# Kernel optimization log

Hardware: AMD Instinct MI355X
Metric: run time of the kernel (lower is better)

## Reference

```python
import jax, jax.numpy as jnp
import numpy as np

N_NODES = 50000
N_EDGES = 800000
D_IN = 64
D_OUT = 64


def setup_inputs() -> dict:
    key = jax.random.key(0)
    k1, k2, k3, k4 = jax.random.split(key, 4)
    x = jax.random.normal(k1, (N_NODES, D_IN), dtype=jnp.float32)
    W = jax.random.normal(k2, (D_IN, D_OUT), dtype=jnp.float32) / np.sqrt(D_IN)
    bias = jnp.zeros((D_OUT,), dtype=jnp.float32)
    # learned per-edge weights (AdaptiveEdgeWeightGNN.edge_attr, initialized from fixed_values)
    edge_weight = jax.random.uniform(k3, (N_EDGES,), dtype=jnp.float32)
    edge_index = jax.random.randint(k4, (2, N_EDGES), 0, N_NODES, dtype=jnp.int64)
    return {"x": x, "W": W, "bias": bias, "edge_weight": edge_weight, "edge_index": edge_index}


def reference(x, W, bias, edge_weight, edge_index):
    # PyG GCNConv forward: gcn_norm (add self-loops, symmetric normalization
    # using the edge weights), linear transform, gather-scale-scatter, + bias.
    N = x.shape[0]
    row = edge_index[0]  # source nodes
    col = edge_index[1]  # target nodes
    loop = jnp.arange(N, dtype=edge_index.dtype)
    row = jnp.concatenate([row, loop])
    col = jnp.concatenate([col, loop])
    ew = jnp.concatenate([edge_weight, jnp.ones((N,), dtype=edge_weight.dtype)])
    # degree from edge weights scattered onto target nodes
    deg = jax.ops.segment_sum(ew, col, num_segments=N)
    deg_inv_sqrt = jnp.where(deg > 0, jax.lax.rsqrt(deg), 0.0)
    norm = deg_inv_sqrt[row] * ew * deg_inv_sqrt[col]  # [E+N]
    xw = x @ W  # [N, D_OUT]
    msgs = xw[row] * norm[:, None]  # gather + scale
    out = jax.ops.segment_sum(msgs, col, num_segments=N)  # scatter-add
    return out + bias
```

## Files before the change

kernel.cpp:

```cpp
#include <hip/hip_runtime.h>

#define N_NODES 50000
#define N_EDGES 800000
#define D 64
#define NCHUNK 64
#define CHUNK_E (N_EDGES / NCHUNK)
#define NRANGE 4
#define RANGE_N 16384
#define PAD 8
#define REC_CAP (N_EDGES + (PAD - 1) * N_NODES)
#define NB_NODE 196
#define PLACE_BLOCKS (N_EDGES / 256)

typedef int iv4 __attribute__((ext_vector_type(4)));

__device__ __forceinline__ unsigned short f2bf(float f) {
    unsigned int u = __float_as_uint(f);
    u += 0x7FFFu + ((u >> 16) & 1u);
    return (unsigned short)(u >> 16);
}
__device__ __forceinline__ float bf2f(unsigned int s) {
    return __uint_as_float(s << 16);
}

__global__ __launch_bounds__(1024) void k_hist(const int* __restrict__ col,
                                               unsigned short* __restrict__ part,
                                               unsigned short* __restrict__ lrank) {
    __shared__ unsigned int h[RANGE_N / 2];
    int i = blockIdx.x >> 2;
    int j = blockIdx.x & 3;
    int t = threadIdx.x;
    for (int k = t; k < RANGE_N / 2; k += 1024) h[k] = 0;
    __syncthreads();
    int base = i * CHUNK_E;
    for (int e = base + t; e < base + CHUNK_E; e += 1024) {
        int c = col[e];
        if ((c >> 14) == j) {
            int local = c & (RANGE_N - 1);
            int sh = (local & 1) << 4;
            unsigned int lr = atomicAdd(&h[local >> 1], 1u << sh);
            lrank[e] = (unsigned short)((lr >> sh) & 0xffffu);
        }
    }
    __syncthreads();
    for (int k = t; k < RANGE_N; k += 1024) {
        int n = j * RANGE_N + k;
        if (n < N_NODES)
            part[(size_t)i * N_NODES + n] =
                (unsigned short)((h[k >> 1] >> ((k & 1) << 4)) & 0xffffu);
    }
}

__global__ __launch_bounds__(256) void k_scan(unsigned short* __restrict__ part,
                                              int* __restrict__ start,
                                              int* __restrict__ cnttot,
                                              int* __restrict__ partials) {
    __shared__ int s[256];
    int b = blockIdx.x, t = threadIdx.x;
    int n = b * 256 + t;
    unsigned int run = 0;
    if (n < N_NODES) {
#pragma unroll 8
        for (int i = 0; i < NCHUNK; ++i) {
            size_t idx = (size_t)i * N_NODES + n;
            unsigned int v = part[idx];
            part[idx] = (unsigned short)run;
            run += v;
        }
        cnttot[n] = (int)run;
    }
    int cnt = (n < N_NODES) ? (int)((run + PAD - 1) & ~(unsigned)(PAD - 1)) : 0;
    s[t] = cnt;
    __syncthreads();
    for (int off = 1; off < 256; off <<= 1) {
        int a = (t >= off) ? s[t - off] : 0;
        __syncthreads();
        s[t] += a;
        __syncthreads();
    }
    if (n <= N_NODES) start[n] = s[t] - cnt;
    if (t == 255) partials[b] = s[255];
}

__global__ __launch_bounds__(256) void k_scanfin(int* __restrict__ start,
                                                 const int* __restrict__ partials) {
    __shared__ int red[256];
    int b = blockIdx.x, t = threadIdx.x;
    red[t] = (t < b) ? partials[t] : 0;
    __syncthreads();
    for (int off = 128; off > 0; off >>= 1) {
        if (t < off) red[t] += red[t + off];
        __syncthreads();
    }
    int offset = red[0];
    int n = b * 256 + t;
    if (n <= N_NODES) start[n] += offset;
}

__global__ __launch_bounds__(256) void k_place(const int* __restrict__ ei,
                                               const float* __restrict__ ew,
                                               const int* __restrict__ start,
                                               const int* __restrict__ cnttot,
                                               const unsigned short* __restrict__ part,
                                               const unsigned short* __restrict__ lrank,
                                               unsigned int* __restrict__ rec) {
    int b = blockIdx.x, t = threadIdx.x;
    if (b < PLACE_BLOCKS) {
        int e = b * 256 + t;
        int c = ei[N_EDGES + e];
        int i = e / CHUNK_E;
        int pos = start[c] + (int)part[(size_t)i * N_NODES + c] + (int)lrank[e];
        rec[pos] = (unsigned int)ei[e] | ((unsigned int)f2bf(ew[e]) << 16);
    } else {
        int n = (b - PLACE_BLOCKS) * 256 + t;
        if (n < N_NODES) {
            int j = start[n] + cnttot[n];
            int j1 = start[n + 1];
            for (; j < j1; ++j) rec[j] = 0u;
        }
    }
}

__global__ __launch_bounds__(256) void k_deg(const int* __restrict__ start,
                                             const unsigned int* __restrict__ rec,
                                             float* __restrict__ dis) {
    int wave = threadIdx.x >> 6;
    int lane = threadIdx.x & 63;
    int n = blockIdx.x * 4 + wave;
    int j0 = start[n], j1 = start[n + 1];
    float s = 0.0f;
    for (int j = j0 + lane; j < j1; j += 64) s += bf2f(rec[j] >> 16);
    for (int off = 32; off > 0; off >>= 1) s += __shfl_down(s, off);
    if (lane == 0) dis[n] = rsqrtf(1.0f + s);
}

__global__ __launch_bounds__(256, 4) void k_xw(const float* __restrict__ x,
                                               const float* __restrict__ W,
                                               const float* __restrict__ dis,
                                               unsigned short* __restrict__ xw16) {
    __shared__ float Ws[64 * 64];
    int t = threadIdx.x;
    for (int i = t; i < 1024; i += 256)
        ((float4*)Ws)[i] = ((const float4*)W)[i];
    __syncthreads();

    int cg = t & 15;
    int rg = t >> 4;
    int r0 = blockIdx.x * 64;
    int ra = min(r0 + rg,      N_NODES - 1);
    int rb = min(r0 + rg + 16, N_NODES - 1);
    int rc = min(r0 + rg + 32, N_NODES - 1);
    int rd = min(r0 + rg + 48, N_NODES - 1);
    const float4* x4 = (const float4*)x;

    float4 acc0 = make_float4(0.f, 0.f, 0.f, 0.f);
    float4 acc1 = acc0, acc2 = acc0, acc3 = acc0;

#pragma unroll 1
    for (int k4 = 0; k4 < 16; ++k4) {
        float4 xv0 = x4[ra * 16 + k4];
        float4 xv1 = x4[rb * 16 + k4];
        float4 xv2 = x4[rc * 16 + k4];
        float4 xv3 = x4[rd * 16 + k4];
        float4 w0 = *(const float4*)&Ws[(k4 * 4 + 0) * 64 + cg * 4];
        float4 w1 = *(const float4*)&Ws[(k4 * 4 + 1) * 64 + cg * 4];
        float4 w2 = *(const float4*)&Ws[(k4 * 4 + 2) * 64 + cg * 4];
        float4 w3 = *(const float4*)&Ws[(k4 * 4 + 3) * 64 + cg * 4];
        acc0.x = fmaf(xv0.x, w0.x, acc0.x); acc0.y = fmaf(xv0.x, w0.y, acc0.y);
        acc0.z = fmaf(xv0.x, w0.z, acc0.z); acc0.w = fmaf(xv0.x, w0.w, acc0.w);
        acc0.x = fmaf(xv0.y, w1.x, acc0.x); acc0.y = fmaf(xv0.y, w1.y, acc0.y);
        acc0.z = fmaf(xv0.y, w1.z, acc0.z); acc0.w = fmaf(xv0.y, w1.w, acc0.w);
        acc0.x = fmaf(xv0.z, w2.x, acc0.x); acc0.y = fmaf(xv0.z, w2.y, acc0.y);
        acc0.z = fmaf(xv0.z, w2.z, acc0.z); acc0.w = fmaf(xv0.z, w2.w, acc0.w);
        acc0.x = fmaf(xv0.w, w3.x, acc0.x); acc0.y = fmaf(xv0.w, w3.y, acc0.y);
        acc0.z = fmaf(xv0.w, w3.z, acc0.z); acc0.w = fmaf(xv0.w, w3.w, acc0.w);
        acc1.x = fmaf(xv1.x, w0.x, acc1.x); acc1.y = fmaf(xv1.x, w0.y, acc1.y);
        acc1.z = fmaf(xv1.x, w0.z, acc1.z); acc1.w = fmaf(xv1.x, w0.w, acc1.w);
        acc1.x = fmaf(xv1.y, w1.x, acc1.x); acc1.y = fmaf(xv1.y, w1.y, acc1.y);
        acc1.z = fmaf(xv1.y, w1.z, acc1.z); acc1.w = fmaf(xv1.y, w1.w, acc1.w);
        acc1.x = fmaf(xv1.z, w2.x, acc1.x); acc1.y = fmaf(xv1.z, w2.y, acc1.y);
        acc1.z = fmaf(xv1.z, w2.z, acc1.z); acc1.w = fmaf(xv1.z, w2.w, acc1.w);
        acc1.x = fmaf(xv1.w, w3.x, acc1.x); acc1.y = fmaf(xv1.w, w3.y, acc1.y);
        acc1.z = fmaf(xv1.w, w3.z, acc1.z); acc1.w = fmaf(xv1.w, w3.w, acc1.w);
        acc2.x = fmaf(xv2.x, w0.x, acc2.x); acc2.y = fmaf(xv2.x, w0.y, acc2.y);
        acc2.z = fmaf(xv2.x, w0.z, acc2.z); acc2.w = fmaf(xv2.x, w0.w, acc2.w);
        acc2.x = fmaf(xv2.y, w1.x, acc2.x); acc2.y = fmaf(xv2.y, w1.y, acc2.y);
        acc2.z = fmaf(xv2.y, w1.z, acc2.z); acc2.w = fmaf(xv2.y, w1.w, acc2.w);
        acc2.x = fmaf(xv2.z, w2.x, acc2.x); acc2.y = fmaf(xv2.z, w2.y, acc2.y);
        acc2.z = fmaf(xv2.z, w2.z, acc2.z); acc2.w = fmaf(xv2.z, w2.w, acc2.w);
        acc2.x = fmaf(xv2.w, w3.x, acc2.x); acc2.y = fmaf(xv2.w, w3.y, acc2.y);
        acc2.z = fmaf(xv2.w, w3.z, acc2.z); acc2.w = fmaf(xv2.w, w3.w, acc2.w);
        acc3.x = fmaf(xv3.x, w0.x, acc3.x); acc3.y = fmaf(xv3.x, w0.y, acc3.y);
        acc3.z = fmaf(xv3.x, w0.z, acc3.z); acc3.w = fmaf(xv3.x, w0.w, acc3.w);
        acc3.x = fmaf(xv3.y, w1.x, acc3.x); acc3.y = fmaf(xv3.y, w1.y, acc3.y);
        acc3.z = fmaf(xv3.y, w1.z, acc3.z); acc3.w = fmaf(xv3.y, w1.w, acc3.w);
        acc3.x = fmaf(xv3.z, w2.x, acc3.x); acc3.y = fmaf(xv3.z, w2.y, acc3.y);
        acc3.z = fmaf(xv3.z, w2.z, acc3.z); acc3.w = fmaf(xv3.z, w2.w, acc3.w);
        acc3.x = fmaf(xv3.w, w3.x, acc3.x); acc3.y = fmaf(xv3.w, w3.y, acc3.y);
        acc3.z = fmaf(xv3.w, w3.z, acc3.z); acc3.w = fmaf(xv3.w, w3.w, acc3.w);
    }

    float4 accs[4] = { acc0, acc1, acc2, acc3 };
#pragma unroll
    for (int i = 0; i < 4; ++i) {
        int row = r0 + rg + 16 * i;
        if (row < N_NODES) {
            float s = dis[row];
            ushort4 s4 = make_ushort4(f2bf(accs[i].x * s), f2bf(accs[i].y * s),
                                      f2bf(accs[i].z * s), f2bf(accs[i].w * s));
            *(ushort4*)&xw16[row * 64 + cg * 4] = s4;
        }
    }
}

__global__ __launch_bounds__(256) void k_gather(const int* __restrict__ start,
                                                const unsigned int* __restrict__ rec,
                                                const unsigned short* __restrict__ xw16,
                                                const float* __restrict__ dis,
                                                const float* __restrict__ bias,
                                                float* __restrict__ out) {
    int wave = threadIdx.x >> 6;
    int c = threadIdx.x & 63;
    int n = blockIdx.x * 4 + wave;
    float di = dis[n];
    float acc[8];
#pragma unroll
    for (int k = 0; k < 8; ++k) acc[k] = 0.f;
    acc[0] = bf2f((unsigned int)xw16[n * 64 + c]);
    int j0 = start[n], j1 = start[n + 1];
    int iters = (j1 - j0) >> 3;
    const iv4* rq = (const iv4*)(rec + j0);
    iv4 q0 = rq[0], q1 = rq[1];
    for (int it = 0; it < iters; ++it) {
        iv4 p0 = q0, p1 = q1;
        q0 = rq[2 * it + 2];
        q1 = rq[2 * it + 3];
        unsigned int r[8] = { (unsigned int)p0.x, (unsigned int)p0.y,
                              (unsigned int)p0.z, (unsigned int)p0.w,
                              (unsigned int)p1.x, (unsigned int)p1.y,
                              (unsigned int)p1.z, (unsigned int)p1.w };
        float v[8];
#pragma unroll
        for (int k = 0; k < 8; ++k)
            v[k] = bf2f((unsigned int)xw16[(r[k] & 0xffffu) * 64 + c]);
#pragma unroll
        for (int k = 0; k < 8; ++k)
            acc[k] = fmaf(v[k], bf2f(r[k] >> 16), acc[k]);
    }
    float a = ((acc[0] + acc[1]) + (acc[2] + acc[3])) + ((acc[4] + acc[5]) + (acc[6] + acc[7]));
    out[n * 64 + c] = fmaf(a, di, bias[c]);
}

extern "C" void kernel_launch(void* const* d_in, const int* in_sizes, int n_in,
                              void* d_out, int out_size, void* d_ws, size_t ws_size,
                              hipStream_t stream) {
    const float* x    = (const float*)d_in[0];
    const float* W    = (const float*)d_in[1];
    const float* bias = (const float*)d_in[2];
    const float* ew   = (const float*)d_in[3];
    const int*   ei   = (const int*)d_in[4];
    float* out = (float*)d_out;

    char* wsb = (char*)d_ws;
    unsigned int*   rec   = (unsigned int*)wsb;
    unsigned short* xw16  = (unsigned short*)(wsb + 6200000);
    unsigned short* lrank = (unsigned short*)(wsb + 12600000);
    unsigned short* part  = (unsigned short*)(wsb + 14200000);
    float*          dis   = (float*)(wsb + 20600000);
    int*            cnttot= (int*)(wsb + 20800000);
    int*            start = (int*)(wsb + 21000000);
    int*            partials = (int*)(wsb + 21200016);

    k_hist<<<NCHUNK * NRANGE, 1024, 0, stream>>>(ei + N_EDGES, part, lrank);
    k_scan<<<NB_NODE, 256, 0, stream>>>(part, start, cnttot, partials);
    k_scanfin<<<NB_NODE, 256, 0, stream>>>(start, partials);
    k_place<<<PLACE_BLOCKS + NB_NODE, 256, 0, stream>>>(ei, ew, start, cnttot, part, lrank, rec);
    k_deg<<<N_NODES / 4, 256, 0, stream>>>(start, rec, dis);
    k_xw<<<(N_NODES + 63) / 64, 256, 0, stream>>>(x, W, dis, xw16);
    k_gather<<<N_NODES / 4, 256, 0, stream>>>(start, rec, xw16, dis, bias, out);
}
```

Before: 88.11 us.

## Fuse scan passes via decoupled lookback, drop padding, fold degree into xw

```diff
diff --git a/kernel.cpp b/kernel.cpp
--- a/kernel.cpp
+++ b/kernel.cpp
@@ -7,10 +7,9 @@
 #define CHUNK_E (N_EDGES / NCHUNK)
 #define NRANGE 4
 #define RANGE_N 16384
-#define PAD 8
-#define REC_CAP (N_EDGES + (PAD - 1) * N_NODES)
 #define NB_NODE 196
 #define PLACE_BLOCKS (N_EDGES / 256)
+#define FLAGBIT 0x80000000u
 
 typedef int iv4 __attribute__((ext_vector_type(4)));
 
@@ -25,11 +24,13 @@
 
 __global__ __launch_bounds__(1024) void k_hist(const int* __restrict__ col,
                                                unsigned short* __restrict__ part,
-                                               unsigned short* __restrict__ lrank) {
+                                               unsigned short* __restrict__ lrank,
+                                               unsigned int* __restrict__ partials) {
     __shared__ unsigned int h[RANGE_N / 2];
     int i = blockIdx.x >> 2;
     int j = blockIdx.x & 3;
     int t = threadIdx.x;
+    if (blockIdx.x == 0 && t < 256) partials[t] = 0;
     for (int k = t; k < RANGE_N / 2; k += 1024) h[k] = 0;
     __syncthreads();
     int base = i * CHUNK_E;
@@ -53,9 +54,9 @@
 
 __global__ __launch_bounds__(256) void k_scan(unsigned short* __restrict__ part,
                                               int* __restrict__ start,
-                                              int* __restrict__ cnttot,
-                                              int* __restrict__ partials) {
+                                              unsigned int* __restrict__ partials) {
     __shared__ int s[256];
+    __shared__ int red[256];
     int b = blockIdx.x, t = threadIdx.x;
     int n = b * 256 + t;
     unsigned int run = 0;
@@ -67,9 +68,8 @@
             part[idx] = (unsigned short)run;
             run += v;
         }
-        cnttot[n] = (int)run;
-    }
-    int cnt = (n < N_NODES) ? (int)((run + PAD - 1) & ~(unsigned)(PAD - 1)) : 0;
+    }
+    int cnt = (n < N_NODES) ? (int)run : 0;
     s[t] = cnt;
     __syncthreads();
     for (int off = 1; off < 256; off <<= 1) {
@@ -78,75 +78,73 @@
         s[t] += a;
         __syncthreads();
     }
-    if (n <= N_NODES) start[n] = s[t] - cnt;
-    if (t == 255) partials[b] = s[255];
-}
-
-__global__ __launch_bounds__(256) void k_scanfin(int* __restrict__ start,
-                                                 const int* __restrict__ partials) {
-    __shared__ int red[256];
-    int b = blockIdx.x, t = threadIdx.x;
-    red[t] = (t < b) ? partials[t] : 0;
+    if (t == 255)
+        __hip_atomic_store(&partials[b], (unsigned int)s[255] | FLAGBIT,
+                           __ATOMIC_RELEASE, __HIP_MEMORY_SCOPE_AGENT);
+    unsigned int pv = 0;
+    if (t < b) {
+        unsigned int v;
+        do {
+            v = __hip_atomic_load(&partials[t], __ATOMIC_ACQUIRE, __HIP_MEMORY_SCOPE_AGENT);
+        } while (!(v & FLAGBIT));
+        pv = v & ~FLAGBIT;
+    }
+    red[t] = (int)pv;
     __syncthreads();
     for (int off = 128; off > 0; off >>= 1) {
         if (t < off) red[t] += red[t + off];
         __syncthreads();
     }
     int offset = red[0];
-    int n = b * 256 + t;
-    if (n <= N_NODES) start[n] += offset;
+    if (n <= N_NODES) start[n] = offset + s[t] - cnt;
 }
 
 __global__ __launch_bounds__(256) void k_place(const int* __restrict__ ei,
                                                const float* __restrict__ ew,
                                                const int* __restrict__ start,
-                                               const int* __restrict__ cnttot,
                                                const unsigned short* __restrict__ part,
                                                const unsigned short* __restrict__ lrank,
                                                unsigned int* __restrict__ rec) {
-    int b = blockIdx.x, t = threadIdx.x;
-    if (b < PLACE_BLOCKS) {
-        int e = b * 256 + t;
-        int c = ei[N_EDGES + e];
-        int i = e / CHUNK_E;
-        int pos = start[c] + (int)part[(size_t)i * N_NODES + c] + (int)lrank[e];
-        rec[pos] = (unsigned int)ei[e] | ((unsigned int)f2bf(ew[e]) << 16);
-    } else {
-        int n = (b - PLACE_BLOCKS) * 256 + t;
-        if (n < N_NODES) {
-            int j = start[n] + cnttot[n];
-            int j1 = start[n + 1];
-            for (; j < j1; ++j) rec[j] = 0u;
-        }
-    }
-}
-
-__global__ __launch_bounds__(256) void k_deg(const int* __restrict__ start,
-                                             const unsigned int* __restrict__ rec,
-                                             float* __restrict__ dis) {
-    int wave = threadIdx.x >> 6;
-    int lane = threadIdx.x & 63;
-    int n = blockIdx.x * 4 + wave;
-    int j0 = start[n], j1 = start[n + 1];
-    float s = 0.0f;
-    for (int j = j0 + lane; j < j1; j += 64) s += bf2f(rec[j] >> 16);
-    for (int off = 32; off > 0; off >>= 1) s += __shfl_down(s, off);
-    if (lane == 0) dis[n] = rsqrtf(1.0f + s);
+    int e = blockIdx.x * 256 + threadIdx.x;
+    int c = ei[N_EDGES + e];
+    int i = e / CHUNK_E;
+    int pos = start[c] + (int)part[(size_t)i * N_NODES + c] + (int)lrank[e];
+    rec[pos] = (unsigned int)ei[e] | ((unsigned int)f2bf(ew[e]) << 16);
 }
 
 __global__ __launch_bounds__(256, 4) void k_xw(const float* __restrict__ x,
                                                const float* __restrict__ W,
-                                               const float* __restrict__ dis,
+                                               const int* __restrict__ start,
+                                               const unsigned int* __restrict__ rec,
+                                               float* __restrict__ dis,
                                                unsigned short* __restrict__ xw16) {
     __shared__ float Ws[64 * 64];
+    __shared__ float dls[64];
     int t = threadIdx.x;
+    int r0 = blockIdx.x * 64;
     for (int i = t; i < 1024; i += 256)
         ((float4*)Ws)[i] = ((const float4*)W)[i];
+
+    {
+        int q = t >> 2, l = t & 3;
+        int node = r0 + q;
+        float s = 0.f;
+        if (node < N_NODES) {
+            int j0 = start[node], j1 = start[node + 1];
+            for (int j = j0 + l; j < j1; j += 4) s += bf2f(rec[j] >> 16);
+        }
+        s += __shfl_xor(s, 1);
+        s += __shfl_xor(s, 2);
+        if (l == 0 && node < N_NODES) {
+            float dv = rsqrtf(1.0f + s);
+            dls[q] = dv;
+            dis[node] = dv;
+        }
+    }
     __syncthreads();
 
     int cg = t & 15;
     int rg = t >> 4;
-    int r0 = blockIdx.x * 64;
     int ra = min(r0 + rg,      N_NODES - 1);
     int rb = min(r0 + rg + 16, N_NODES - 1);
     int rc = min(r0 + rg + 32, N_NODES - 1);
@@ -205,7 +203,7 @@
     for (int i = 0; i < 4; ++i) {
         int row = r0 + rg + 16 * i;
         if (row < N_NODES) {
-            float s = dis[row];
+            float s = dls[rg + 16 * i];
             ushort4 s4 = make_ushort4(f2bf(accs[i].x * s), f2bf(accs[i].y * s),
                                       f2bf(accs[i].z * s), f2bf(accs[i].w * s));
             *(ushort4*)&xw16[row * 64 + cg * 4] = s4;
@@ -227,14 +225,16 @@
 #pragma unroll
     for (int k = 0; k < 8; ++k) acc[k] = 0.f;
     acc[0] = bf2f((unsigned int)xw16[n * 64 + c]);
-    int j0 = start[n], j1 = start[n + 1];
-    int iters = (j1 - j0) >> 3;
+    int j0 = start[n];
+    int cnt = start[n + 1] - j0;
+    int nit = (cnt + 7) >> 3;
     const iv4* rq = (const iv4*)(rec + j0);
     iv4 q0 = rq[0], q1 = rq[1];
-    for (int it = 0; it < iters; ++it) {
+    for (int it = 0; it < nit; ++it) {
         iv4 p0 = q0, p1 = q1;
         q0 = rq[2 * it + 2];
         q1 = rq[2 * it + 3];
+        int rem = cnt - (it << 3);
         unsigned int r[8] = { (unsigned int)p0.x, (unsigned int)p0.y,
                               (unsigned int)p0.z, (unsigned int)p0.w,
                               (unsigned int)p1.x, (unsigned int)p1.y,
@@ -244,8 +244,10 @@
         for (int k = 0; k < 8; ++k)
             v[k] = bf2f((unsigned int)xw16[(r[k] & 0xffffu) * 64 + c]);
 #pragma unroll
-        for (int k = 0; k < 8; ++k)
-            acc[k] = fmaf(v[k], bf2f(r[k] >> 16), acc[k]);
+        for (int k = 0; k < 8; ++k) {
+            float w = (k < rem) ? bf2f(r[k] >> 16) : 0.0f;
+            acc[k] = fmaf(v[k], w, acc[k]);
+        }
     }
     float a = ((acc[0] + acc[1]) + (acc[2] + acc[3])) + ((acc[4] + acc[5]) + (acc[6] + acc[7]));
     out[n * 64 + c] = fmaf(a, di, bias[c]);
@@ -267,15 +269,12 @@
     unsigned short* lrank = (unsigned short*)(wsb + 12600000);
     unsigned short* part  = (unsigned short*)(wsb + 14200000);
     float*          dis   = (float*)(wsb + 20600000);
-    int*            cnttot= (int*)(wsb + 20800000);
     int*            start = (int*)(wsb + 21000000);
-    int*            partials = (int*)(wsb + 21200016);
-
-    k_hist<<<NCHUNK * NRANGE, 1024, 0, stream>>>(ei + N_EDGES, part, lrank);
-    k_scan<<<NB_NODE, 256, 0, stream>>>(part, start, cnttot, partials);
-    k_scanfin<<<NB_NODE, 256, 0, stream>>>(start, partials);
-    k_place<<<PLACE_BLOCKS + NB_NODE, 256, 0, stream>>>(ei, ew, start, cnttot, part, lrank, rec);
-    k_deg<<<N_NODES / 4, 256, 0, stream>>>(start, rec, dis);
-    k_xw<<<(N_NODES + 63) / 64, 256, 0, stream>>>(x, W, dis, xw16);
+    unsigned int*   partials = (unsigned int*)(wsb + 21300000);
+
+    k_hist<<<NCHUNK * NRANGE, 1024, 0, stream>>>(ei + N_EDGES, part, lrank, partials);
+    k_scan<<<NB_NODE, 256, 0, stream>>>(part, start, partials);
+    k_place<<<PLACE_BLOCKS, 256, 0, stream>>>(ei, ew, start, part, lrank, rec);
+    k_xw<<<(N_NODES + 63) / 64, 256, 0, stream>>>(x, W, start, rec, dis, xw16);
     k_gather<<<N_NODES / 4, 256, 0, stream>>>(start, rec, xw16, dis, bias, out);
 }
```

Result: no change. 87.95 us (-0.2%).
